# Optimization experiments

Hardware: AMD Instinct MI355X
Metric: run time of the kernel (lower is better)

Reference implementation:

```python
import jax, jax.numpy as jnp
import numpy as np

B, S, D, H, E = 4, 2048, 1024, 2048, 8  # batch, seq, input_dim, hidden_dim, num_experts(=world_size)


def setup_inputs() -> dict:
    key = jax.random.key(0)
    ks = jax.random.split(key, 8)
    scale = 0.02
    return {
        "x": jax.random.normal(ks[0], (B, S, D), dtype=jnp.float32),
        "Wr": jax.random.normal(ks[1], (D, E), dtype=jnp.float32) * scale,
        "br": jnp.zeros((E,), dtype=jnp.float32),
        "W1": jax.random.normal(ks[2], (E, D, H), dtype=jnp.float32) * scale,
        "b1": jnp.zeros((E, H), dtype=jnp.float32),
        "W2": jax.random.normal(ks[3], (E, H, D), dtype=jnp.float32) * scale,
        "b2": jnp.zeros((E, D), dtype=jnp.float32),
    }


def reference(x, Wr, br, W1, b1, W2, b2):
    # Single-process equivalent of the expert-parallel layer: token t is
    # processed by the MLP of the rank/expert it is routed to (top-1 router),
    # then scaled by its routing probability. all-to-all + sort/unsort is a
    # permutation and cancels out mathematically.
    d = x.shape[-1]
    tokens = x.reshape(-1, d)                               # [T, D]
    logits = tokens @ Wr + br                               # [T, E]
    probs = jax.nn.softmax(logits, axis=-1)
    expert = jnp.argmax(probs, axis=-1)                     # [T] int, top-1 dest
    max_prob = jnp.take_along_axis(probs, expert[:, None], axis=-1)  # [T, 1]
    # dense per-expert MLP then select the routed expert's output per token
    h = jax.nn.relu(jnp.einsum("td,edh->teh", tokens, W1) + b1[None])  # [T, E, H]
    y = jnp.einsum("teh,ehd->ted", h, W2) + b2[None]                   # [T, E, D]
    out = jnp.take_along_axis(y, expert[:, None, None], axis=1)[:, 0, :]  # [T, D]
    return (out * max_prob).reshape(x.shape)
```

## Files before the change

kernel.cpp:

```cpp
#include <hip/hip_runtime.h>
#include <hip/hip_bf16.h>
#include <stdint.h>


typedef unsigned short bf16_t;
typedef short short8 __attribute__((ext_vector_type(8)));
typedef float f32x4 __attribute__((ext_vector_type(4)));

#define T_TOK 8192
#define DDIM 1024
#define HDIM 2048
#define NEXP 8
#define MAXT64 136
#define ROWSP (MAXT64 * 64)

__device__ __forceinline__ bf16_t f2b(float f) {
    unsigned int x = __builtin_bit_cast(unsigned int, f);
    unsigned int r = x + 0x7fffu + ((x >> 16) & 1u);
    return (bf16_t)(r >> 16);
}
__device__ __forceinline__ void gld_lds16(const bf16_t* src, bf16_t* dst) {
    __builtin_amdgcn_global_load_lds((const __attribute__((address_space(1))) void*)src,
                                     (__attribute__((address_space(3))) void*)dst, 16, 0, 0);
}

__global__ __launch_bounds__(256) void router_kernel(
    const float* __restrict__ x, const float* __restrict__ Wr,
    const float* __restrict__ br, int* __restrict__ expert_id,
    float* __restrict__ gate, int* __restrict__ counts,
    bf16_t* __restrict__ xbf) {
    __shared__ int hcnt[NEXP];
    int tid = threadIdx.x, wave = tid >> 6, lane = tid & 63;
    if (tid < NEXP) hcnt[tid] = 0;
    __syncthreads();

    float w[4][4][NEXP];
#pragma unroll
    for (int i = 0; i < 4; i++)
#pragma unroll
        for (int j = 0; j < 4; j++) {
            const float* p = Wr + (size_t)(i * 256 + lane * 4 + j) * NEXP;
            float4 a = *(const float4*)p;
            float4 b = *(const float4*)(p + 4);
            w[i][j][0] = a.x; w[i][j][1] = a.y; w[i][j][2] = a.z; w[i][j][3] = a.w;
            w[i][j][4] = b.x; w[i][j][5] = b.y; w[i][j][6] = b.z; w[i][j][7] = b.w;
        }

    int t0 = (blockIdx.x * 4 + wave) * 4;
#pragma unroll
    for (int tt = 0; tt < 4; tt++) {
        int t = t0 + tt;
        float acc[NEXP];
#pragma unroll
        for (int e = 0; e < NEXP; e++) acc[e] = 0.f;
#pragma unroll
        for (int i = 0; i < 4; i++) {
            const float* xp = x + (size_t)t * DDIM + i * 256 + lane * 4;
            float4 xv = *(const float4*)xp;
            bf16_t tmp[4] = {f2b(xv.x), f2b(xv.y), f2b(xv.z), f2b(xv.w)};
            *(uint2*)(xbf + (size_t)t * DDIM + i * 256 + lane * 4) = *(uint2*)tmp;
            float xs[4] = {xv.x, xv.y, xv.z, xv.w};
#pragma unroll
            for (int j = 0; j < 4; j++)
#pragma unroll
                for (int e = 0; e < NEXP; e++) acc[e] += xs[j] * w[i][j][e];
        }
#pragma unroll
        for (int off = 32; off; off >>= 1)
#pragma unroll
            for (int e = 0; e < NEXP; e++) acc[e] += __shfl_xor(acc[e], off);
        if (lane == 0) {
            float l[NEXP];
#pragma unroll
            for (int e = 0; e < NEXP; e++) l[e] = acc[e] + br[e];
            int best = 0; float bm = l[0];
#pragma unroll
            for (int e = 1; e < NEXP; e++) if (l[e] > bm) { bm = l[e]; best = e; }
            float s = 0.f;
#pragma unroll
            for (int e = 0; e < NEXP; e++) s += __expf(l[e] - bm);
            expert_id[t] = best;
            gate[t] = 1.0f / s;
            atomicAdd(&hcnt[best], 1);
        }
    }
    __syncthreads();
    if (tid < NEXP) atomicAdd(&counts[tid], hcnt[tid]);
}

__global__ __launch_bounds__(256) void scan_kernel(const int* __restrict__ counts,
                                                   int* __restrict__ pad_off,
                                                   int* __restrict__ tile_expert,
                                                   int* __restrict__ tok_of_row) {
    for (int i = threadIdx.x; i < ROWSP; i += 256) tok_of_row[i] = -1;
    if (threadIdx.x == 0) {
        int rowoff = 0, t = 0;
        for (int e = 0; e < NEXP; e++) {
            pad_off[e] = rowoff;
            int nt = (counts[e] + 63) >> 6;
            rowoff += nt << 6;
            for (int i = 0; i < nt; i++) tile_expert[t++] = e;
        }
        while (t < MAXT64) tile_expert[t++] = -1;
    }
}

__global__ __launch_bounds__(256) void scatter_kernel(
    const int* __restrict__ expert_id, const float* __restrict__ gate,
    const int* __restrict__ pad_off, int* __restrict__ cursor,
    int* __restrict__ tok_of_row, float* __restrict__ gate_of_row) {
    int t = blockIdx.x * 256 + threadIdx.x;
    int e = expert_id[t];
    int p = atomicAdd(&cursor[e], 1);
    int row = pad_off[e] + p;
    tok_of_row[row] = t;
    gate_of_row[row] = gate[t];
}

__global__ __launch_bounds__(256) void transpose_all_kernel(
    const float* __restrict__ W1, const float* __restrict__ W2,
    bf16_t* __restrict__ W1t, bf16_t* __restrict__ W2t) {
    __shared__ bf16_t tile[64][72];
    int z = blockIdx.z;
    const float* inp; bf16_t* outp; int R, C;
    if (z < 8) { inp = W1 + (size_t)z * DDIM * HDIM; outp = W1t + (size_t)z * DDIM * HDIM;
                 R = DDIM; C = HDIM; }
    else       { inp = W2 + (size_t)(z - 8) * HDIM * DDIM; outp = W2t + (size_t)(z - 8) * HDIM * DDIM;
                 R = HDIM; C = DDIM; }
    int ctiles = C >> 6;
    int cx = blockIdx.x % ctiles, ry = blockIdx.x / ctiles;
    int r0 = ry * 64, c0 = cx * 64;
    int tid = threadIdx.x;
#pragma unroll
    for (int v = tid; v < 1024; v += 256) {
        int r = v >> 4, c = (v & 15) * 4;
        float4 f = *(const float4*)(inp + (size_t)(r0 + r) * C + c0 + c);
        tile[r][c + 0] = f2b(f.x); tile[r][c + 1] = f2b(f.y);
        tile[r][c + 2] = f2b(f.z); tile[r][c + 3] = f2b(f.w);
    }
    __syncthreads();
#pragma unroll
    for (int v = tid; v < 512; v += 256) {
        int c = v >> 3, r = (v & 7) * 8;
        bf16_t tmp[8];
#pragma unroll
        for (int i = 0; i < 8; i++) tmp[i] = tile[r + i][c];
        *(uint4*)(outp + (size_t)(c0 + c) * R + r0 + r) = *(uint4*)tmp;
    }
}

__global__ __launch_bounds__(256) void gemm1_kernel(
    const bf16_t* __restrict__ x, const bf16_t* __restrict__ W1t,
    const float* __restrict__ b1, const int* __restrict__ tile_expert,
    const int* __restrict__ tok_of_row, bf16_t* __restrict__ hbuf) {
    constexpr int K = DDIM, N = HDIM;
    int tile_n = blockIdx.x, tile_m = blockIdx.y;
    int e = tile_expert[tile_m];
    if (e < 0) return;
    __shared__ bf16_t lA[64 * 64];
    __shared__ bf16_t lB[128 * 64];
    int tid = threadIdx.x, wave = tid >> 6, lane = tid & 63;
    int sc = (lane & 7) ^ ((lane >> 3) & 7);
    const bf16_t* asrc[2]; const bf16_t* bsrc[4];
#pragma unroll
    for (int c = 0; c < 2; c++) {
        int rr = wave * 16 + c * 8 + (lane >> 3);
        int tok = tok_of_row[tile_m * 64 + rr];
        if (tok < 0) tok = 0;
        asrc[c] = x + (size_t)tok * K + sc * 8;
    }
#pragma unroll
    for (int c = 0; c < 4; c++) {
        int rr = wave * 32 + c * 8 + (lane >> 3);
        bsrc[c] = W1t + (size_t)e * N * K + (size_t)(tile_n * 128 + rr) * K + sc * 8;
    }
    f32x4 acc[2][4];
#pragma unroll
    for (int i = 0; i < 2; i++)
#pragma unroll
        for (int j = 0; j < 4; j++) acc[i][j] = {0.f, 0.f, 0.f, 0.f};
    int wm = wave >> 1, wn = wave & 1;
    int lm = lane & 15, quad = lane >> 4;
    int sw = lm & 7;
    for (int k0 = 0; k0 < K; k0 += 64) {
        __syncthreads();
#pragma unroll
        for (int c = 0; c < 2; c++)
            gld_lds16(asrc[c] + k0, &lA[(wave * 16 + c * 8) * 64]);
#pragma unroll
        for (int c = 0; c < 4; c++)
            gld_lds16(bsrc[c] + k0, &lB[(wave * 32 + c * 8) * 64]);
        __syncthreads();
#pragma unroll
        for (int kk = 0; kk < 2; kk++) {
            int slot = ((kk * 4 + quad) ^ sw) * 8;
            short8 a[2], b[4];
#pragma unroll
            for (int i = 0; i < 2; i++)
                a[i] = *(const short8*)&lA[(wm * 32 + i * 16 + lm) * 64 + slot];
#pragma unroll
            for (int j = 0; j < 4; j++)
                b[j] = *(const short8*)&lB[(wn * 64 + j * 16 + lm) * 64 + slot];
#pragma unroll
            for (int i = 0; i < 2; i++)
#pragma unroll
                for (int j = 0; j < 4; j++)
                    acc[i][j] = __builtin_amdgcn_mfma_f32_16x16x32_bf16(a[i], b[j], acc[i][j], 0, 0, 0);
        }
    }
#pragma unroll
    for (int j = 0; j < 4; j++) {
        int col = tile_n * 128 + wn * 64 + j * 16 + lm;
        float bias = b1[e * N + col];
#pragma unroll
        for (int i = 0; i < 2; i++)
#pragma unroll
            for (int r = 0; r < 4; r++) {
                int row = tile_m * 64 + wm * 32 + i * 16 + quad * 4 + r;
                float v = acc[i][j][r] + bias;
                hbuf[(size_t)row * N + col] = f2b(fmaxf(v, 0.f));
            }
    }
}

__global__ __launch_bounds__(256) void gemm2_kernel(
    const bf16_t* __restrict__ hbuf, const bf16_t* __restrict__ W2t,
    const float* __restrict__ b2, const int* __restrict__ tile_expert,
    const int* __restrict__ tok_of_row, const float* __restrict__ gate_of_row,
    float* __restrict__ out) {
    constexpr int K = HDIM, N = DDIM;
    int tile_n = blockIdx.x, tile_m = blockIdx.y;
    int e = tile_expert[tile_m];
    if (e < 0) return;
    __shared__ bf16_t lA[64 * 64];
    __shared__ bf16_t lB[128 * 64];
    int tid = threadIdx.x, wave = tid >> 6, lane = tid & 63;
    int sc = (lane & 7) ^ ((lane >> 3) & 7);
    const bf16_t* asrc[2]; const bf16_t* bsrc[4];
#pragma unroll
    for (int c = 0; c < 2; c++) {
        int rr = wave * 16 + c * 8 + (lane >> 3);
        asrc[c] = hbuf + (size_t)(tile_m * 64 + rr) * K + sc * 8;
    }
#pragma unroll
    for (int c = 0; c < 4; c++) {
        int rr = wave * 32 + c * 8 + (lane >> 3);
        bsrc[c] = W2t + (size_t)e * N * K + (size_t)(tile_n * 128 + rr) * K + sc * 8;
    }
    f32x4 acc[2][4];
#pragma unroll
    for (int i = 0; i < 2; i++)
#pragma unroll
        for (int j = 0; j < 4; j++) acc[i][j] = {0.f, 0.f, 0.f, 0.f};
    int wm = wave >> 1, wn = wave & 1;
    int lm = lane & 15, quad = lane >> 4;
    int sw = lm & 7;
    for (int k0 = 0; k0 < K; k0 += 64) {
        __syncthreads();
#pragma unroll
        for (int c = 0; c < 2; c++)
            gld_lds16(asrc[c] + k0, &lA[(wave * 16 + c * 8) * 64]);
#pragma unroll
        for (int c = 0; c < 4; c++)
            gld_lds16(bsrc[c] + k0, &lB[(wave * 32 + c * 8) * 64]);
        __syncthreads();
#pragma unroll
        for (int kk = 0; kk < 2; kk++) {
            int slot = ((kk * 4 + quad) ^ sw) * 8;
            short8 a[2], b[4];
#pragma unroll
            for (int i = 0; i < 2; i++)
                a[i] = *(const short8*)&lA[(wm * 32 + i * 16 + lm) * 64 + slot];
#pragma unroll
            for (int j = 0; j < 4; j++)
                b[j] = *(const short8*)&lB[(wn * 64 + j * 16 + lm) * 64 + slot];
#pragma unroll
            for (int i = 0; i < 2; i++)
#pragma unroll
                for (int j = 0; j < 4; j++)
                    acc[i][j] = __builtin_amdgcn_mfma_f32_16x16x32_bf16(a[i], b[j], acc[i][j], 0, 0, 0);
        }
    }
#pragma unroll
    for (int j = 0; j < 4; j++) {
        int col = tile_n * 128 + wn * 64 + j * 16 + lm;
        float bias = b2[e * N + col];
#pragma unroll
        for (int i = 0; i < 2; i++)
#pragma unroll
            for (int r = 0; r < 4; r++) {
                int row = tile_m * 64 + wm * 32 + i * 16 + quad * 4 + r;
                int tok = tok_of_row[row];
                if (tok >= 0) {
                    float v = (acc[i][j][r] + bias) * gate_of_row[row];
                    out[(size_t)tok * N + col] = v;
                }
            }
    }
}

extern "C" void kernel_launch(void* const* d_in, const int* in_sizes, int n_in,
                              void* d_out, int out_size, void* d_ws, size_t ws_size,
                              hipStream_t stream) {
    const float* x  = (const float*)d_in[0];
    const float* Wr = (const float*)d_in[1];
    const float* br = (const float*)d_in[2];
    const float* W1 = (const float*)d_in[3];
    const float* b1 = (const float*)d_in[4];
    const float* W2 = (const float*)d_in[5];
    const float* b2 = (const float*)d_in[6];
    float* out = (float*)d_out;
    char* ws = (char*)d_ws;

    int*    counts      = (int*)(ws + 0);
    int*    cursor      = (int*)(ws + 32);
    int*    pad_off     = (int*)(ws + 64);
    int*    tile_expert = (int*)(ws + 96);
    int*    expert_id   = (int*)(ws + 1024);
    float*  gate        = (float*)(ws + 33792);
    int*    tok_of_row  = (int*)(ws + 66560);
    float*  gate_of_row = (float*)(ws + 101376);
    bf16_t* hbuf        = (bf16_t*)(ws + 136192);
    bf16_t* W1t         = (bf16_t*)(ws + 35787776);
    bf16_t* W2t         = (bf16_t*)(ws + 69342208);
    bf16_t* xbf         = (bf16_t*)(ws + 102896640);

    hipMemsetAsync(counts, 0, 64, stream);

    router_kernel<<<512, 256, 0, stream>>>(x, Wr, br, expert_id, gate, counts, xbf);
    scan_kernel<<<1, 256, 0, stream>>>(counts, pad_off, tile_expert, tok_of_row);
    scatter_kernel<<<T_TOK / 256, 256, 0, stream>>>(expert_id, gate, pad_off, cursor,
                                                    tok_of_row, gate_of_row);
    transpose_all_kernel<<<dim3(512, 1, 16), 256, 0, stream>>>(W1, W2, W1t, W2t);
    gemm1_kernel<<<dim3(HDIM / 128, MAXT64), 256, 0, stream>>>(xbf, W1t, b1, tile_expert,
                                                               tok_of_row, hbuf);
    gemm2_kernel<<<dim3(DDIM / 128, MAXT64), 256, 0, stream>>>(hbuf, W2t, b2, tile_expert,
                                                               tok_of_row, gate_of_row, out);
}
```

Measured before the change: 389.1 us.

## Enlarge grouped GEMM M-tiles to 128 rows with per-tile base and row counts

Both expert GEMMs move from 64x128 to 128x128 block tiles. Each wave now computes a 64x64 sub-tile with 16 MFMA accumulators, which raises reuse of each loaded B fragment and halves the number of M-tile blocks. The scan kernel now emits a base row and a valid row count per tile, so 64-row padded expert segments can end in a half-filled 128-row tile, and epilogue stores skip rows past the count. The tok_of_row initialisation moves from a single-block loop to a memset. In exchange, register pressure rises, and partially filled tiles still compute their full 128 rows.

```diff
diff --git a/kernel.cpp b/kernel.cpp
--- a/kernel.cpp
+++ b/kernel.cpp
@@ -11,8 +11,8 @@
 #define DDIM 1024
 #define HDIM 2048
 #define NEXP 8
-#define MAXT64 136
-#define ROWSP (MAXT64 * 64)
+#define ROWSP 8704
+#define MAXT 72
 
 __device__ __forceinline__ bf16_t f2b(float f) {
     unsigned int x = __builtin_bit_cast(unsigned int, f);
@@ -88,20 +88,27 @@
     if (tid < NEXP) atomicAdd(&counts[tid], hcnt[tid]);
 }
 
-__global__ __launch_bounds__(256) void scan_kernel(const int* __restrict__ counts,
-                                                   int* __restrict__ pad_off,
-                                                   int* __restrict__ tile_expert,
-                                                   int* __restrict__ tok_of_row) {
-    for (int i = threadIdx.x; i < ROWSP; i += 256) tok_of_row[i] = -1;
+__global__ __launch_bounds__(64) void scan_kernel(const int* __restrict__ counts,
+                                                  int* __restrict__ pad_off,
+                                                  int* __restrict__ tile_expert,
+                                                  int* __restrict__ tile_base,
+                                                  int* __restrict__ tile_rows) {
     if (threadIdx.x == 0) {
         int rowoff = 0, t = 0;
         for (int e = 0; e < NEXP; e++) {
             pad_off[e] = rowoff;
-            int nt = (counts[e] + 63) >> 6;
-            rowoff += nt << 6;
-            for (int i = 0; i < nt; i++) tile_expert[t++] = e;
-        }
-        while (t < MAXT64) tile_expert[t++] = -1;
+            int nt64 = (counts[e] + 63) >> 6;
+            int segrows = nt64 << 6;
+            for (int i = 0; i < segrows; i += 128) {
+                tile_expert[t] = e;
+                tile_base[t] = rowoff + i;
+                int rem = segrows - i;
+                tile_rows[t] = rem < 128 ? rem : 128;
+                t++;
+            }
+            rowoff += segrows;
+        }
+        while (t < MAXT) { tile_expert[t] = -1; tile_base[t] = 0; tile_rows[t] = 0; t++; }
     }
 }
 
@@ -152,31 +159,30 @@
 __global__ __launch_bounds__(256) void gemm1_kernel(
     const bf16_t* __restrict__ x, const bf16_t* __restrict__ W1t,
     const float* __restrict__ b1, const int* __restrict__ tile_expert,
+    const int* __restrict__ tile_base, const int* __restrict__ tile_rows,
     const int* __restrict__ tok_of_row, bf16_t* __restrict__ hbuf) {
     constexpr int K = DDIM, N = HDIM;
     int tile_n = blockIdx.x, tile_m = blockIdx.y;
     int e = tile_expert[tile_m];
     if (e < 0) return;
-    __shared__ bf16_t lA[64 * 64];
+    int base = tile_base[tile_m], rows = tile_rows[tile_m];
+    __shared__ bf16_t lA[128 * 64];
     __shared__ bf16_t lB[128 * 64];
     int tid = threadIdx.x, wave = tid >> 6, lane = tid & 63;
     int sc = (lane & 7) ^ ((lane >> 3) & 7);
-    const bf16_t* asrc[2]; const bf16_t* bsrc[4];
-#pragma unroll
-    for (int c = 0; c < 2; c++) {
-        int rr = wave * 16 + c * 8 + (lane >> 3);
-        int tok = tok_of_row[tile_m * 64 + rr];
+    const bf16_t* asrc[4]; const bf16_t* bsrc[4];
+#pragma unroll
+    for (int c = 0; c < 4; c++) {
+        int rr = wave * 32 + c * 8 + (lane >> 3);
+        int gr = base + rr; if (gr > ROWSP - 1) gr = ROWSP - 1;
+        int tok = tok_of_row[gr];
         if (tok < 0) tok = 0;
         asrc[c] = x + (size_t)tok * K + sc * 8;
-    }
-#pragma unroll
-    for (int c = 0; c < 4; c++) {
-        int rr = wave * 32 + c * 8 + (lane >> 3);
         bsrc[c] = W1t + (size_t)e * N * K + (size_t)(tile_n * 128 + rr) * K + sc * 8;
     }
-    f32x4 acc[2][4];
-#pragma unroll
-    for (int i = 0; i < 2; i++)
+    f32x4 acc[4][4];
+#pragma unroll
+    for (int i = 0; i < 4; i++)
 #pragma unroll
         for (int j = 0; j < 4; j++) acc[i][j] = {0.f, 0.f, 0.f, 0.f};
     int wm = wave >> 1, wn = wave & 1;
@@ -185,24 +191,22 @@
     for (int k0 = 0; k0 < K; k0 += 64) {
         __syncthreads();
 #pragma unroll
-        for (int c = 0; c < 2; c++)
-            gld_lds16(asrc[c] + k0, &lA[(wave * 16 + c * 8) * 64]);
-#pragma unroll
-        for (int c = 0; c < 4; c++)
+        for (int c = 0; c < 4; c++) {
+            gld_lds16(asrc[c] + k0, &lA[(wave * 32 + c * 8) * 64]);
             gld_lds16(bsrc[c] + k0, &lB[(wave * 32 + c * 8) * 64]);
+        }
         __syncthreads();
 #pragma unroll
         for (int kk = 0; kk < 2; kk++) {
             int slot = ((kk * 4 + quad) ^ sw) * 8;
-            short8 a[2], b[4];
-#pragma unroll
-            for (int i = 0; i < 2; i++)
-                a[i] = *(const short8*)&lA[(wm * 32 + i * 16 + lm) * 64 + slot];
-#pragma unroll
-            for (int j = 0; j < 4; j++)
-                b[j] = *(const short8*)&lB[(wn * 64 + j * 16 + lm) * 64 + slot];
-#pragma unroll
-            for (int i = 0; i < 2; i++)
+            short8 a[4], b[4];
+#pragma unroll
+            for (int i = 0; i < 4; i++) {
+                a[i] = *(const short8*)&lA[(wm * 64 + i * 16 + lm) * 64 + slot];
+                b[i] = *(const short8*)&lB[(wn * 64 + i * 16 + lm) * 64 + slot];
+            }
+#pragma unroll
+            for (int i = 0; i < 4; i++)
 #pragma unroll
                 for (int j = 0; j < 4; j++)
                     acc[i][j] = __builtin_amdgcn_mfma_f32_16x16x32_bf16(a[i], b[j], acc[i][j], 0, 0, 0);
@@ -213,43 +217,44 @@
         int col = tile_n * 128 + wn * 64 + j * 16 + lm;
         float bias = b1[e * N + col];
 #pragma unroll
-        for (int i = 0; i < 2; i++)
+        for (int i = 0; i < 4; i++) {
+            int rl0 = wm * 64 + i * 16 + quad * 4;
+            if (rl0 >= rows) continue;
 #pragma unroll
             for (int r = 0; r < 4; r++) {
-                int row = tile_m * 64 + wm * 32 + i * 16 + quad * 4 + r;
                 float v = acc[i][j][r] + bias;
-                hbuf[(size_t)row * N + col] = f2b(fmaxf(v, 0.f));
-            }
+                hbuf[(size_t)(base + rl0 + r) * N + col] = f2b(fmaxf(v, 0.f));
+            }
+        }
     }
 }
 
 __global__ __launch_bounds__(256) void gemm2_kernel(
     const bf16_t* __restrict__ hbuf, const bf16_t* __restrict__ W2t,
     const float* __restrict__ b2, const int* __restrict__ tile_expert,
+    const int* __restrict__ tile_base, const int* __restrict__ tile_rows,
     const int* __restrict__ tok_of_row, const float* __restrict__ gate_of_row,
     float* __restrict__ out) {
     constexpr int K = HDIM, N = DDIM;
     int tile_n = blockIdx.x, tile_m = blockIdx.y;
     int e = tile_expert[tile_m];
     if (e < 0) return;
-    __shared__ bf16_t lA[64 * 64];
+    int base = tile_base[tile_m], rows = tile_rows[tile_m];
+    __shared__ bf16_t lA[128 * 64];
     __shared__ bf16_t lB[128 * 64];
     int tid = threadIdx.x, wave = tid >> 6, lane = tid & 63;
     int sc = (lane & 7) ^ ((lane >> 3) & 7);
-    const bf16_t* asrc[2]; const bf16_t* bsrc[4];
-#pragma unroll
-    for (int c = 0; c < 2; c++) {
-        int rr = wave * 16 + c * 8 + (lane >> 3);
-        asrc[c] = hbuf + (size_t)(tile_m * 64 + rr) * K + sc * 8;
-    }
+    const bf16_t* asrc[4]; const bf16_t* bsrc[4];
 #pragma unroll
     for (int c = 0; c < 4; c++) {
         int rr = wave * 32 + c * 8 + (lane >> 3);
+        int gr = base + rr; if (gr > ROWSP - 1) gr = ROWSP - 1;
+        asrc[c] = hbuf + (size_t)gr * K + sc * 8;
         bsrc[c] = W2t + (size_t)e * N * K + (size_t)(tile_n * 128 + rr) * K + sc * 8;
     }
-    f32x4 acc[2][4];
-#pragma unroll
-    for (int i = 0; i < 2; i++)
+    f32x4 acc[4][4];
+#pragma unroll
+    for (int i = 0; i < 4; i++)
 #pragma unroll
         for (int j = 0; j < 4; j++) acc[i][j] = {0.f, 0.f, 0.f, 0.f};
     int wm = wave >> 1, wn = wave & 1;
@@ -258,24 +263,22 @@
     for (int k0 = 0; k0 < K; k0 += 64) {
         __syncthreads();
 #pragma unroll
-        for (int c = 0; c < 2; c++)
-            gld_lds16(asrc[c] + k0, &lA[(wave * 16 + c * 8) * 64]);
-#pragma unroll
-        for (int c = 0; c < 4; c++)
+        for (int c = 0; c < 4; c++) {
+            gld_lds16(asrc[c] + k0, &lA[(wave * 32 + c * 8) * 64]);
             gld_lds16(bsrc[c] + k0, &lB[(wave * 32 + c * 8) * 64]);
+        }
         __syncthreads();
 #pragma unroll
         for (int kk = 0; kk < 2; kk++) {
             int slot = ((kk * 4 + quad) ^ sw) * 8;
-            short8 a[2], b[4];
-#pragma unroll
-            for (int i = 0; i < 2; i++)
-                a[i] = *(const short8*)&lA[(wm * 32 + i * 16 + lm) * 64 + slot];
-#pragma unroll
-            for (int j = 0; j < 4; j++)
-                b[j] = *(const short8*)&lB[(wn * 64 + j * 16 + lm) * 64 + slot];
-#pragma unroll
-            for (int i = 0; i < 2; i++)
+            short8 a[4], b[4];
+#pragma unroll
+            for (int i = 0; i < 4; i++) {
+                a[i] = *(const short8*)&lA[(wm * 64 + i * 16 + lm) * 64 + slot];
+                b[i] = *(const short8*)&lB[(wn * 64 + i * 16 + lm) * 64 + slot];
+            }
+#pragma unroll
+            for (int i = 0; i < 4; i++)
 #pragma unroll
                 for (int j = 0; j < 4; j++)
                     acc[i][j] = __builtin_amdgcn_mfma_f32_16x16x32_bf16(a[i], b[j], acc[i][j], 0, 0, 0);
@@ -286,16 +289,19 @@
         int col = tile_n * 128 + wn * 64 + j * 16 + lm;
         float bias = b2[e * N + col];
 #pragma unroll
-        for (int i = 0; i < 2; i++)
+        for (int i = 0; i < 4; i++) {
+            int rl0 = wm * 64 + i * 16 + quad * 4;
+            if (rl0 >= rows) continue;
 #pragma unroll
             for (int r = 0; r < 4; r++) {
-                int row = tile_m * 64 + wm * 32 + i * 16 + quad * 4 + r;
+                int row = base + rl0 + r;
                 int tok = tok_of_row[row];
                 if (tok >= 0) {
                     float v = (acc[i][j][r] + bias) * gate_of_row[row];
                     out[(size_t)tok * N + col] = v;
                 }
             }
+        }
     }
 }
 
@@ -316,24 +322,29 @@
     int*    cursor      = (int*)(ws + 32);
     int*    pad_off     = (int*)(ws + 64);
     int*    tile_expert = (int*)(ws + 96);
-    int*    expert_id   = (int*)(ws + 1024);
-    float*  gate        = (float*)(ws + 33792);
-    int*    tok_of_row  = (int*)(ws + 66560);
-    float*  gate_of_row = (float*)(ws + 101376);
-    bf16_t* hbuf        = (bf16_t*)(ws + 136192);
-    bf16_t* W1t         = (bf16_t*)(ws + 35787776);
-    bf16_t* W2t         = (bf16_t*)(ws + 69342208);
-    bf16_t* xbf         = (bf16_t*)(ws + 102896640);
+    int*    tile_base   = (int*)(ws + 384);
+    int*    tile_rows   = (int*)(ws + 672);
+    int*    expert_id   = (int*)(ws + 960);
+    float*  gate        = (float*)(ws + 33728);
+    int*    tok_of_row  = (int*)(ws + 66496);
+    float*  gate_of_row = (float*)(ws + 101312);
+    bf16_t* hbuf        = (bf16_t*)(ws + 136128);
+    bf16_t* W1t         = (bf16_t*)(ws + 35787712);
+    bf16_t* W2t         = (bf16_t*)(ws + 69342144);
+    bf16_t* xbf         = (bf16_t*)(ws + 102896576);
 
     hipMemsetAsync(counts, 0, 64, stream);
+    hipMemsetAsync(tok_of_row, 0xFF, ROWSP * 4, stream);
 
     router_kernel<<<512, 256, 0, stream>>>(x, Wr, br, expert_id, gate, counts, xbf);
-    scan_kernel<<<1, 256, 0, stream>>>(counts, pad_off, tile_expert, tok_of_row);
+    scan_kernel<<<1, 64, 0, stream>>>(counts, pad_off, tile_expert, tile_base, tile_rows);
     scatter_kernel<<<T_TOK / 256, 256, 0, stream>>>(expert_id, gate, pad_off, cursor,
                                                     tok_of_row, gate_of_row);
     transpose_all_kernel<<<dim3(512, 1, 16), 256, 0, stream>>>(W1, W2, W1t, W2t);
-    gemm1_kernel<<<dim3(HDIM / 128, MAXT64), 256, 0, stream>>>(xbf, W1t, b1, tile_expert,
-                                                               tok_of_row, hbuf);
-    gemm2_kernel<<<dim3(DDIM / 128, MAXT64), 256, 0, stream>>>(hbuf, W2t, b2, tile_expert,
-                                                               tok_of_row, gate_of_row, out);
-}
+    gemm1_kernel<<<dim3(HDIM / 128, MAXT), 256, 0, stream>>>(xbf, W1t, b1, tile_expert,
+                                                             tile_base, tile_rows,
+                                                             tok_of_row, hbuf);
+    gemm2_kernel<<<dim3(DDIM / 128, MAXT), 256, 0, stream>>>(hbuf, W2t, b2, tile_expert,
+                                                             tile_base, tile_rows,
+                                                             tok_of_row, gate_of_row, out);
+}
```

Measured after the change: 460.2 us. +18.3%, slower.

## Double-buffer LDS tiles in expert GEMMs and memset tok_of_row

Applied to the files above, without the earlier changes.

Both expert GEMM kernels now use two LDS buffers and issue the global-to-LDS loads for the next K tile before the MFMAs on the current one. This cuts the per-iteration barrier count from two to one and lets load latency hide behind math. The cost is double the shared memory per block (48KB), which may lower occupancy. Separately, the -1 initialisation of tok_of_row moves out of the single-block scan kernel into a hipMemsetAsync.

```diff
diff --git a/kernel.cpp b/kernel.cpp
--- a/kernel.cpp
+++ b/kernel.cpp
@@ -88,11 +88,9 @@
     if (tid < NEXP) atomicAdd(&counts[tid], hcnt[tid]);
 }
 
-__global__ __launch_bounds__(256) void scan_kernel(const int* __restrict__ counts,
-                                                   int* __restrict__ pad_off,
-                                                   int* __restrict__ tile_expert,
-                                                   int* __restrict__ tok_of_row) {
-    for (int i = threadIdx.x; i < ROWSP; i += 256) tok_of_row[i] = -1;
+__global__ __launch_bounds__(64) void scan_kernel(const int* __restrict__ counts,
+                                                  int* __restrict__ pad_off,
+                                                  int* __restrict__ tile_expert) {
     if (threadIdx.x == 0) {
         int rowoff = 0, t = 0;
         for (int e = 0; e < NEXP; e++) {
@@ -149,6 +147,16 @@
     }
 }
 
+#define STAGE_G(bufA, bufB, k0)                                            \
+    do {                                                                   \
+        _Pragma("unroll")                                                  \
+        for (int c = 0; c < 2; c++)                                        \
+            gld_lds16(asrc[c] + (k0), &(bufA)[(wave * 16 + c * 8) * 64]);  \
+        _Pragma("unroll")                                                  \
+        for (int c = 0; c < 4; c++)                                        \
+            gld_lds16(bsrc[c] + (k0), &(bufB)[(wave * 32 + c * 8) * 64]);  \
+    } while (0)
+
 __global__ __launch_bounds__(256) void gemm1_kernel(
     const bf16_t* __restrict__ x, const bf16_t* __restrict__ W1t,
     const float* __restrict__ b1, const int* __restrict__ tile_expert,
@@ -157,8 +165,8 @@
     int tile_n = blockIdx.x, tile_m = blockIdx.y;
     int e = tile_expert[tile_m];
     if (e < 0) return;
-    __shared__ bf16_t lA[64 * 64];
-    __shared__ bf16_t lB[128 * 64];
+    __shared__ bf16_t lA[2][64 * 64];
+    __shared__ bf16_t lB[2][128 * 64];
     int tid = threadIdx.x, wave = tid >> 6, lane = tid & 63;
     int sc = (lane & 7) ^ ((lane >> 3) & 7);
     const bf16_t* asrc[2]; const bf16_t* bsrc[4];
@@ -182,31 +190,32 @@
     int wm = wave >> 1, wn = wave & 1;
     int lm = lane & 15, quad = lane >> 4;
     int sw = lm & 7;
-    for (int k0 = 0; k0 < K; k0 += 64) {
-        __syncthreads();
-#pragma unroll
-        for (int c = 0; c < 2; c++)
-            gld_lds16(asrc[c] + k0, &lA[(wave * 16 + c * 8) * 64]);
-#pragma unroll
-        for (int c = 0; c < 4; c++)
-            gld_lds16(bsrc[c] + k0, &lB[(wave * 32 + c * 8) * 64]);
-        __syncthreads();
+
+    constexpr int NT = K / 64;
+    STAGE_G(lA[0], lB[0], 0);
+    __syncthreads();
+    int cur = 0;
+    for (int t = 0; t < NT; ++t) {
+        if (t + 1 < NT)
+            STAGE_G(lA[cur ^ 1], lB[cur ^ 1], (t + 1) * 64);
 #pragma unroll
         for (int kk = 0; kk < 2; kk++) {
             int slot = ((kk * 4 + quad) ^ sw) * 8;
             short8 a[2], b[4];
 #pragma unroll
             for (int i = 0; i < 2; i++)
-                a[i] = *(const short8*)&lA[(wm * 32 + i * 16 + lm) * 64 + slot];
+                a[i] = *(const short8*)&lA[cur][(wm * 32 + i * 16 + lm) * 64 + slot];
 #pragma unroll
             for (int j = 0; j < 4; j++)
-                b[j] = *(const short8*)&lB[(wn * 64 + j * 16 + lm) * 64 + slot];
+                b[j] = *(const short8*)&lB[cur][(wn * 64 + j * 16 + lm) * 64 + slot];
 #pragma unroll
             for (int i = 0; i < 2; i++)
 #pragma unroll
                 for (int j = 0; j < 4; j++)
                     acc[i][j] = __builtin_amdgcn_mfma_f32_16x16x32_bf16(a[i], b[j], acc[i][j], 0, 0, 0);
         }
+        __syncthreads();
+        cur ^= 1;
     }
 #pragma unroll
     for (int j = 0; j < 4; j++) {
@@ -232,8 +241,8 @@
     int tile_n = blockIdx.x, tile_m = blockIdx.y;
     int e = tile_expert[tile_m];
     if (e < 0) return;
-    __shared__ bf16_t lA[64 * 64];
-    __shared__ bf16_t lB[128 * 64];
+    __shared__ bf16_t lA[2][64 * 64];
+    __shared__ bf16_t lB[2][128 * 64];
     int tid = threadIdx.x, wave = tid >> 6, lane = tid & 63;
     int sc = (lane & 7) ^ ((lane >> 3) & 7);
     const bf16_t* asrc[2]; const bf16_t* bsrc[4];
@@ -255,31 +264,32 @@
     int wm = wave >> 1, wn = wave & 1;
     int lm = lane & 15, quad = lane >> 4;
     int sw = lm & 7;
-    for (int k0 = 0; k0 < K; k0 += 64) {
-        __syncthreads();
-#pragma unroll
-        for (int c = 0; c < 2; c++)
-            gld_lds16(asrc[c] + k0, &lA[(wave * 16 + c * 8) * 64]);
-#pragma unroll
-        for (int c = 0; c < 4; c++)
-            gld_lds16(bsrc[c] + k0, &lB[(wave * 32 + c * 8) * 64]);
-        __syncthreads();
+
+    constexpr int NT = K / 64;
+    STAGE_G(lA[0], lB[0], 0);
+    __syncthreads();
+    int cur = 0;
+    for (int t = 0; t < NT; ++t) {
+        if (t + 1 < NT)
+            STAGE_G(lA[cur ^ 1], lB[cur ^ 1], (t + 1) * 64);
 #pragma unroll
         for (int kk = 0; kk < 2; kk++) {
             int slot = ((kk * 4 + quad) ^ sw) * 8;
             short8 a[2], b[4];
 #pragma unroll
             for (int i = 0; i < 2; i++)
-                a[i] = *(const short8*)&lA[(wm * 32 + i * 16 + lm) * 64 + slot];
+                a[i] = *(const short8*)&lA[cur][(wm * 32 + i * 16 + lm) * 64 + slot];
 #pragma unroll
             for (int j = 0; j < 4; j++)
-                b[j] = *(const short8*)&lB[(wn * 64 + j * 16 + lm) * 64 + slot];
+                b[j] = *(const short8*)&lB[cur][(wn * 64 + j * 16 + lm) * 64 + slot];
 #pragma unroll
             for (int i = 0; i < 2; i++)
 #pragma unroll
                 for (int j = 0; j < 4; j++)
                     acc[i][j] = __builtin_amdgcn_mfma_f32_16x16x32_bf16(a[i], b[j], acc[i][j], 0, 0, 0);
         }
+        __syncthreads();
+        cur ^= 1;
     }
 #pragma unroll
     for (int j = 0; j < 4; j++) {
@@ -326,9 +336,10 @@
     bf16_t* xbf         = (bf16_t*)(ws + 102896640);
 
     hipMemsetAsync(counts, 0, 64, stream);
+    hipMemsetAsync(tok_of_row, 0xFF, ROWSP * 4, stream);
 
     router_kernel<<<512, 256, 0, stream>>>(x, Wr, br, expert_id, gate, counts, xbf);
-    scan_kernel<<<1, 256, 0, stream>>>(counts, pad_off, tile_expert, tok_of_row);
+    scan_kernel<<<1, 64, 0, stream>>>(counts, pad_off, tile_expert);
     scatter_kernel<<<T_TOK / 256, 256, 0, stream>>>(expert_id, gate, pad_off, cursor,
                                                     tok_of_row, gate_of_row);
     transpose_all_kernel<<<dim3(512, 1, 16), 256, 0, stream>>>(W1, W2, W1t, W2t);
```

Result: no change. 394.1 us (+1.3%).
